# Kernel optimization log

Hardware: AMD Instinct MI355X
Metric: run time of the kernel (lower is better)

The kernel has to match this reference:

```python
import jax, jax.numpy as jnp
import numpy as np

VOCAB, EMBED, HIDDEN = 32000, 256, 512
B, S = 64, 64


def setup_inputs() -> dict:
    key = jax.random.key(0)
    ks = jax.random.split(key, 10)
    target_seq = jax.random.randint(ks[0], (B, S), 0, VOCAB)
    context = jax.random.normal(ks[1], (B, HIDDEN), dtype=jnp.float32)
    h = jax.random.normal(ks[2], (B, HIDDEN), dtype=jnp.float32)
    c = jax.random.normal(ks[3], (B, HIDDEN), dtype=jnp.float32)
    # parameters (torch default-ish init scale)
    emb_table = jax.random.normal(ks[4], (VOCAB, EMBED), dtype=jnp.float32)
    k_lstm = 1.0 / np.sqrt(HIDDEN)
    w_ih = jax.random.uniform(ks[5], (4 * HIDDEN, EMBED + HIDDEN), minval=-k_lstm, maxval=k_lstm, dtype=jnp.float32)
    w_hh = jax.random.uniform(ks[6], (4 * HIDDEN, HIDDEN), minval=-k_lstm, maxval=k_lstm, dtype=jnp.float32)
    b_ih = jax.random.uniform(ks[7], (4 * HIDDEN,), minval=-k_lstm, maxval=k_lstm, dtype=jnp.float32)
    b_hh = jnp.zeros((4 * HIDDEN,), dtype=jnp.float32)
    k_fc = 1.0 / np.sqrt(2 * HIDDEN)
    w_fc = jax.random.uniform(ks[8], (VOCAB, 2 * HIDDEN), minval=-k_fc, maxval=k_fc, dtype=jnp.float32)
    b_fc = jax.random.uniform(ks[9], (VOCAB,), minval=-k_fc, maxval=k_fc, dtype=jnp.float32)
    return dict(target_seq=target_seq, context=context, h=h, c=c,
                emb_table=emb_table, w_ih=w_ih, w_hh=w_hh, b_ih=b_ih, b_hh=b_hh,
                w_fc=w_fc, b_fc=b_fc)


def _decode(target_seq, context, h, c, emb_table, w_ih, w_hh, b_ih, b_hh, w_fc, b_fc):
    # teacher_forcing_ratio = 1.0 -> input at step t is target_seq[:, t]
    emb = emb_table[target_seq]                                    # [B,S,E]
    ctx_t = jnp.broadcast_to(context[:, None, :], (emb.shape[0], emb.shape[1], context.shape[1]))
    lstm_in = jnp.concatenate([emb, ctx_t], axis=-1)               # [B,S,E+H]
    # precompute input-to-hidden part of gates for all steps
    pre = jnp.einsum('bsf,gf->bsg', lstm_in, w_ih) + b_ih + b_hh   # [B,S,4H]
    H = h.shape[1]

    def step(carry, pre_t):
        h_t, c_t = carry
        gates = pre_t + h_t @ w_hh.T                               # [B,4H]
        i, f, g, o = jnp.split(gates, 4, axis=-1)
        i, f, o = jax.nn.sigmoid(i), jax.nn.sigmoid(f), jax.nn.sigmoid(o)
        g = jnp.tanh(g)
        c_n = f * c_t + i * g
        h_n = o * jnp.tanh(c_n)
        return (h_n, c_n), h_n

    _, hs = jax.lax.scan(step, (h, c), jnp.swapaxes(pre, 0, 1))    # hs: [S,B,H]
    hs = jnp.swapaxes(hs, 0, 1)                                    # [B,S,H]
    out_in = jnp.concatenate([hs, ctx_t], axis=-1)                 # [B,S,2H]
    logits = jnp.einsum('bsf,vf->bsv', out_in, w_fc) + b_fc        # [B,S,V]
    return logits


def reference(target_seq, context, h, c, emb_table, w_ih, w_hh, b_ih, b_hh, w_fc, b_fc):
    return _decode(target_seq, context, h, c, emb_table, w_ih, w_hh, b_ih, b_hh, w_fc, b_fc)
```

## Files before the change

### kernel.cpp

```cpp
#include <hip/hip_runtime.h>
#include <hip/hip_bf16.h>

#define VOCAB 32000
#define EMBED 256
#define HIDDEN 512
#define BB 64
#define SS 64
#define M_ROWS (BB * SS)
#define G4 (4 * HIDDEN)
#define NBLK 16

typedef __attribute__((ext_vector_type(8))) short short8v;
typedef __attribute__((ext_vector_type(4))) float float4v;
typedef __attribute__((ext_vector_type(4))) unsigned int uint4v;

__device__ __forceinline__ ushort f2bf(float f) {
    union { float f; unsigned u; } v; v.f = f;
    unsigned r = (v.u + 0x7FFFu + ((v.u >> 16) & 1u)) >> 16;
    return (ushort)r;
}

__device__ __forceinline__ float fast_tanh(float x) {
    float xc = fminf(fmaxf(x, -15.f), 15.f);
    float e = __expf(2.f * xc);
    return (e - 1.f) / (e + 1.f);
}

__device__ __forceinline__ void glds16(const ushort* g, ushort* l) {
    __builtin_amdgcn_global_load_lds(
        (const __attribute__((address_space(1))) unsigned int*)(const void*)g,
        (__attribute__((address_space(3))) unsigned int*)(void*)l, 16, 0, 0);
}

__global__ void k_conv_strided(const float* __restrict__ in, ushort* __restrict__ out,
                               int lg2cols, int instride, int n8) {
    int i = blockIdx.x * blockDim.x + threadIdx.x;
    int stride = gridDim.x * blockDim.x;
    int colmask = (1 << lg2cols) - 1;
    for (; i < n8; i += stride) {
        int i8 = i << 3;
        int row = i8 >> lg2cols, col = i8 & colmask;
        const float* src = in + (size_t)row * instride + col;
        float4 v0 = *(const float4*)src;
        float4 v1 = *(const float4*)(src + 4);
        short8v o;
        o[0] = (short)f2bf(v0.x); o[1] = (short)f2bf(v0.y);
        o[2] = (short)f2bf(v0.z); o[3] = (short)f2bf(v0.w);
        o[4] = (short)f2bf(v1.x); o[5] = (short)f2bf(v1.y);
        o[6] = (short)f2bf(v1.z); o[7] = (short)f2bf(v1.w);
        *(short8v*)(out + i8) = o;
    }
}

__global__ void k_build_emb(const int* __restrict__ tseq, const float* __restrict__ emb,
                            ushort* __restrict__ embbf) {
    int rid = blockIdx.x * 8 + (threadIdx.x >> 5);
    int c0 = (threadIdx.x & 31) * 8;
    int tok = tseq[rid];
    const float* src = emb + (size_t)tok * EMBED + c0;
    float4 v0 = *(const float4*)src;
    float4 v1 = *(const float4*)(src + 4);
    short8v o;
    o[0] = (short)f2bf(v0.x); o[1] = (short)f2bf(v0.y);
    o[2] = (short)f2bf(v0.z); o[3] = (short)f2bf(v0.w);
    o[4] = (short)f2bf(v1.x); o[5] = (short)f2bf(v1.y);
    o[6] = (short)f2bf(v1.z); o[7] = (short)f2bf(v1.w);
    *(short8v*)(embbf + (size_t)rid * EMBED + c0) = o;
}

__global__ void k_prep_small(const float* __restrict__ b_ih, const float* __restrict__ b_hh,
                             float* __restrict__ bias_pre,
                             const float* __restrict__ h0, ushort* __restrict__ hbufA,
                             const float* __restrict__ ctx, ushort* __restrict__ ctx_bf,
                             unsigned* __restrict__ ctrl) {
    int i = blockIdx.x * blockDim.x + threadIdx.x;
    if (i < 256) ctrl[i] = 0;
    if (i < G4) bias_pre[i] = b_ih[i] + b_hh[i];
    if (i < BB * HIDDEN) {
        hbufA[i] = f2bf(h0[i]);
        ctx_bf[i] = f2bf(ctx[i]);
    }
}

__global__ __launch_bounds__(256) void k_gemm_smallM(
    const ushort* __restrict__ Abf, const float* __restrict__ Wf, int wstride,
    const float* __restrict__ bias, float* __restrict__ Cout, int N) {
    int t = threadIdx.x;
    int wv = t >> 6, lane = t & 63, lr = lane & 15, kg = lane >> 4;
    int bcol = blockIdx.x * 128;

    float4v acc[4][2];
#pragma unroll
    for (int m = 0; m < 4; m++)
#pragma unroll
        for (int n = 0; n < 2; n++) acc[m][n] = (float4v){0.f, 0.f, 0.f, 0.f};

#pragma unroll 4
    for (int ks = 0; ks < 16; ks++) {
        short8v a[4];
#pragma unroll
        for (int m = 0; m < 4; m++)
            a[m] = *(const short8v*)(Abf + (size_t)(m * 16 + lr) * 512 + ks * 32 + kg * 8);
        short8v w[2];
#pragma unroll
        for (int n = 0; n < 2; n++) {
            const float* src = Wf + (size_t)(bcol + wv * 32 + n * 16 + lr) * wstride + ks * 32 + kg * 8;
            float4 v0 = *(const float4*)src;
            float4 v1 = *(const float4*)(src + 4);
            short8v w8;
            w8[0] = (short)f2bf(v0.x); w8[1] = (short)f2bf(v0.y);
            w8[2] = (short)f2bf(v0.z); w8[3] = (short)f2bf(v0.w);
            w8[4] = (short)f2bf(v1.x); w8[5] = (short)f2bf(v1.y);
            w8[6] = (short)f2bf(v1.z); w8[7] = (short)f2bf(v1.w);
            w[n] = w8;
        }
#pragma unroll
        for (int m = 0; m < 4; m++)
#pragma unroll
            for (int n = 0; n < 2; n++)
                acc[m][n] = __builtin_amdgcn_mfma_f32_16x16x32_bf16(a[m], w[n], acc[m][n], 0, 0, 0);
    }

#pragma unroll
    for (int n = 0; n < 2; n++) {
        int col = bcol + wv * 32 + n * 16 + lr;
        float bv = bias[col];
#pragma unroll
        for (int m = 0; m < 4; m++) {
            int row = m * 16 + kg * 4;
#pragma unroll
            for (int j = 0; j < 4; j++)
                Cout[(size_t)(row + j) * N + col] = acc[m][n][j] + bv;
        }
    }
}

__global__ __launch_bounds__(512) void k_gemm_bf16(
    const ushort* __restrict__ A, const ushort* __restrict__ W,
    const float* __restrict__ rowbias, float* __restrict__ C,
    int M, int N, int K) {
    __shared__ ushort As[256 * 32];
    __shared__ ushort Ws[256 * 32];
    int t = threadIdx.x;

    int gx = N >> 8, gy = M >> 8;
    int nwg = gx * gy;
    int q = nwg >> 3, r = nwg & 7;
    int xcd = blockIdx.x & 7, idx = blockIdx.x >> 3;
    int wg = (xcd < r) ? xcd * (q + 1) + idx : r * (q + 1) + (xcd - r) * q + idx;
    const int SG = 4;
    int grp = wg / (gx * SG);
    int rem = wg % (gx * SG);
    int bx = rem / SG;
    int by = grp * SG + rem % SG;
    int brow = by * 256, bcol = bx * 256;

    int wave = t >> 6, lane = t & 63;
    int wr = wave >> 2, wc = wave & 3;
    int lr = lane & 15, kg = lane >> 4;

    float4v acc[8][4];
#pragma unroll
    for (int m = 0; m < 8; m++)
#pragma unroll
        for (int n = 0; n < 4; n++) acc[m][n] = (float4v){0.f, 0.f, 0.f, 0.f};

    int srow = t >> 2;
    int scol = (((t & 3) ^ (srow & 3))) * 8;
    const ushort* AgA = A + (size_t)(brow + srow) * K + scol;
    const ushort* AgB = A + (size_t)(brow + 128 + srow) * K + scol;
    const ushort* WgA = W + (size_t)(bcol + srow) * K + scol;
    const ushort* WgB = W + (size_t)(bcol + 128 + srow) * K + scol;
    ushort* ldsA0 = &As[(wave * 16) * 32];
    ushort* ldsA1 = &As[(128 + wave * 16) * 32];
    ushort* ldsW0 = &Ws[(wave * 16) * 32];
    ushort* ldsW1 = &Ws[(128 + wave * 16) * 32];

    for (int bk = 0; bk < K; bk += 32) {
        glds16(AgA + bk, ldsA0);
        glds16(AgB + bk, ldsA1);
        glds16(WgA + bk, ldsW0);
        glds16(WgB + bk, ldsW1);
        __syncthreads();
        short8v a[8], w[4];
#pragma unroll
        for (int m = 0; m < 8; m++) {
            int row = wr * 128 + m * 16 + lr;
            a[m] = *(const short8v*)&As[row * 32 + (kg ^ (row & 3)) * 8];
        }
#pragma unroll
        for (int n = 0; n < 4; n++) {
            int row = wc * 64 + n * 16 + lr;
            w[n] = *(const short8v*)&Ws[row * 32 + (kg ^ (row & 3)) * 8];
        }
#pragma unroll
        for (int m = 0; m < 8; m++)
#pragma unroll
            for (int n = 0; n < 4; n++)
                acc[m][n] = __builtin_amdgcn_mfma_f32_16x16x32_bf16(a[m], w[n], acc[m][n], 0, 0, 0);
        __syncthreads();
    }

#pragma unroll
    for (int n = 0; n < 4; n++) {
        int col = bcol + wc * 64 + n * 16 + lr;
#pragma unroll
        for (int m = 0; m < 8; m++) {
            int row = brow + wr * 128 + m * 16 + kg * 4;
            float bv = rowbias[(size_t)(row >> 6) * N + col];
            float4v v = acc[m][n];
#pragma unroll
            for (int j = 0; j < 4; j++)
                C[(size_t)(row + j) * N + col] = v[j] + bv;
        }
    }
}

__global__ __launch_bounds__(512) void k_lstm(
    const float* __restrict__ pre, const float* __restrict__ w_hh,
    const float* __restrict__ c0,
    ushort* __restrict__ hbufA, ushort* __restrict__ hbufB,
    ushort* __restrict__ out_in, unsigned* __restrict__ flags) {
    __shared__ ushort h_lds[64 * HIDDEN];
    __shared__ float G2[64 * 132];
    int p = blockIdx.x;
    int t = threadIdx.x;
    int w = t >> 6, lane = t & 63, lr = lane & 15, kg = lane >> 4;
    int mh = w >> 2, cw2 = w & 3;

    short8v wfrag[2][16];
#pragma unroll
    for (int ci = 0; ci < 2; ci++) {
        const float* wrow = w_hh + (size_t)(cw2 * HIDDEN + p * 32 + ci * 16 + lr) * HIDDEN;
#pragma unroll
        for (int ks = 0; ks < 16; ks++) {
            const float* src = wrow + ks * 32 + kg * 8;
            short8v w8;
#pragma unroll
            for (int e = 0; e < 8; e++) w8[e] = (short)f2bf(src[e]);
            wfrag[ci][ks] = w8;
        }
    }

    int b = t >> 3, jj0 = (t & 7) * 4, jg0 = p * 32 + jj0;
    float4v c_reg = *(const float4v*)(c0 + (size_t)b * HIDDEN + jg0);
    float4v pv[4];
#pragma unroll
    for (int qg = 0; qg < 4; qg++)
        pv[qg] = *(const float4v*)(pre + (size_t)(b * SS) * G4 + qg * HIDDEN + jg0);

    char* hl = (char*)h_lds;

    for (int s = 0; s < SS; s++) {
        const ushort* hb = (s & 1) ? hbufB : hbufA;
        ushort* hn = (s & 1) ? hbufA : hbufB;

        if (s > 0) {
            const unsigned* fp = flags + (lane & 15) * 16;
            unsigned fv;
            do {
                fv = __hip_atomic_load(fp, __ATOMIC_RELAXED, __HIP_MEMORY_SCOPE_AGENT);
            } while (__all((int)(fv >= (unsigned)s)) == 0);
        }

        {
            uint4v vb[8];
#pragma unroll
            for (int i = 0; i < 8; i++) {
                int rr = w * 8 + i;
                const void* src = hb + (size_t)rr * HIDDEN + lane * 8;
                asm volatile("global_load_dwordx4 %0, %1, off sc0 sc1"
                             : "=&v"(vb[i]) : "v"(src));
            }
            asm volatile("s_waitcnt vmcnt(0)" ::: "memory");
#pragma unroll
            for (int i = 0; i < 8; i++) {
                int rr = w * 8 + i;
                int off = (rr * 1024 + lane * 16) ^ ((rr & 7) << 4);
                *(uint4v*)(hl + off) = vb[i];
            }
        }
        __syncthreads();

        float4v acc[2][2];
#pragma unroll
        for (int mi = 0; mi < 2; mi++)
#pragma unroll
            for (int ci = 0; ci < 2; ci++) acc[mi][ci] = (float4v){0.f, 0.f, 0.f, 0.f};
#pragma unroll
        for (int ks = 0; ks < 16; ks++) {
            short8v a[2];
#pragma unroll
            for (int mi = 0; mi < 2; mi++) {
                int row = mh * 32 + mi * 16 + lr;
                int off = (row * 1024 + ks * 64 + kg * 16) ^ ((row & 7) << 4);
                a[mi] = *(const short8v*)(hl + off);
            }
#pragma unroll
            for (int mi = 0; mi < 2; mi++)
#pragma unroll
                for (int ci = 0; ci < 2; ci++)
                    acc[mi][ci] = __builtin_amdgcn_mfma_f32_16x16x32_bf16(a[mi], wfrag[ci][ks], acc[mi][ci], 0, 0, 0);
        }
#pragma unroll
        for (int mi = 0; mi < 2; mi++)
#pragma unroll
            for (int ci = 0; ci < 2; ci++)
#pragma unroll
                for (int rr = 0; rr < 4; rr++)
                    G2[(mh * 32 + mi * 16 + kg * 4 + rr) * 132 + cw2 * 32 + ci * 16 + lr] = acc[mi][ci][rr];
        __syncthreads();

        {
            float4v gq[4];
#pragma unroll
            for (int qg = 0; qg < 4; qg++) gq[qg] = *(const float4v*)&G2[b * 132 + qg * 32 + jj0];
            unsigned long long hv8 = 0;
#pragma unroll
            for (int e = 0; e < 4; e++) {
                float xi = gq[0][e] + pv[0][e];
                float xf = gq[1][e] + pv[1][e];
                float xg = gq[2][e] + pv[2][e];
                float xo = gq[3][e] + pv[3][e];
                float ig = 1.f / (1.f + __expf(-xi));
                float fg = 1.f / (1.f + __expf(-xf));
                float gg = fast_tanh(xg);
                float og = 1.f / (1.f + __expf(-xo));
                float cn = fg * c_reg[e] + ig * gg;
                float hv = og * fast_tanh(cn);
                c_reg[e] = cn;
                hv8 |= (unsigned long long)f2bf(hv) << (16 * e);
            }
            if (s + 1 < SS) {
                __hip_atomic_store((unsigned long long*)(hn + (size_t)b * HIDDEN + jg0), hv8,
                                   __ATOMIC_RELAXED, __HIP_MEMORY_SCOPE_AGENT);
            }
            *(unsigned long long*)(out_in + (size_t)(b * SS + s) * HIDDEN + jg0) = hv8;
            if (s + 1 < SS) {
#pragma unroll
                for (int qg = 0; qg < 4; qg++)
                    pv[qg] = *(const float4v*)(pre + (size_t)(b * SS + s + 1) * G4 + qg * HIDDEN + jg0);
            }
        }

        __syncthreads();
        if (t == 0 && s + 1 < SS)
            __hip_atomic_store(flags + p * 16, (unsigned)(s + 1),
                               __ATOMIC_RELEASE, __HIP_MEMORY_SCOPE_AGENT);
    }
}

extern "C" void kernel_launch(void* const* d_in, const int* in_sizes, int n_in,
                              void* d_out, int out_size, void* d_ws, size_t ws_size,
                              hipStream_t stream) {
    const int*   tseq = (const int*)d_in[0];
    const float* ctx  = (const float*)d_in[1];
    const float* h0   = (const float*)d_in[2];
    const float* c0   = (const float*)d_in[3];
    const float* emb  = (const float*)d_in[4];
    const float* w_ih = (const float*)d_in[5];
    const float* w_hh = (const float*)d_in[6];
    const float* b_ih = (const float*)d_in[7];
    const float* b_hh = (const float*)d_in[8];
    const float* w_fc = (const float*)d_in[9];
    const float* b_fc = (const float*)d_in[10];
    float* out = (float*)d_out;

    char* wsb = (char*)d_ws;
    size_t off = 0;
    auto alloc = [&](size_t bytes) -> void* {
        void* ptr = wsb + off;
        off = (off + bytes + 255) & ~(size_t)255;
        return ptr;
    };
    ushort* emb_bf    = (ushort*)alloc((size_t)M_ROWS * EMBED * 2);
    ushort* w_ih_ebf  = (ushort*)alloc((size_t)G4 * EMBED * 2);
    ushort* w_fc_hbf  = (ushort*)alloc((size_t)VOCAB * HIDDEN * 2);
    ushort* out_in    = (ushort*)alloc((size_t)M_ROWS * HIDDEN * 2);
    float*  pre       = (float*)alloc((size_t)M_ROWS * G4 * 4);
    float*  prectx    = (float*)alloc((size_t)BB * G4 * 4);
    float*  ctxdot    = (float*)alloc((size_t)BB * VOCAB * 4);
    ushort* ctx_bf    = (ushort*)alloc((size_t)BB * HIDDEN * 2);
    ushort* hbufA     = (ushort*)alloc((size_t)BB * HIDDEN * 2);
    ushort* hbufB     = (ushort*)alloc((size_t)BB * HIDDEN * 2);
    float*  bias_pre  = (float*)alloc((size_t)G4 * 4);
    unsigned* ctrl    = (unsigned*)alloc(1024);

    k_conv_strided<<<256, 256, 0, stream>>>(w_ih, w_ih_ebf, 8, 768, G4 * EMBED / 8);
    k_conv_strided<<<2048, 256, 0, stream>>>(w_fc, w_fc_hbf, 9, 1024, VOCAB * HIDDEN / 8);
    k_build_emb<<<M_ROWS / 8, 256, 0, stream>>>(tseq, emb, emb_bf);
    k_prep_small<<<128, 256, 0, stream>>>(b_ih, b_hh, bias_pre, h0, hbufA, ctx, ctx_bf, ctrl);

    k_gemm_smallM<<<G4 / 128, 256, 0, stream>>>(ctx_bf, w_ih + 256, 768, bias_pre, prectx, G4);
    k_gemm_smallM<<<VOCAB / 128, 256, 0, stream>>>(ctx_bf, w_fc + 512, 1024, b_fc, ctxdot, VOCAB);

    k_gemm_bf16<<<dim3((G4 / 256) * (M_ROWS / 256)), 512, 0, stream>>>(
        emb_bf, w_ih_ebf, prectx, pre, M_ROWS, G4, EMBED);

    void* args[] = {(void*)&pre, (void*)&w_hh, (void*)&c0,
                    (void*)&hbufA, (void*)&hbufB, (void*)&out_in, (void*)&ctrl};
    hipLaunchCooperativeKernel((void*)k_lstm, dim3(NBLK), dim3(512), args, 0, stream);

    k_gemm_bf16<<<dim3((VOCAB / 256) * (M_ROWS / 256)), 512, 0, stream>>>(
        out_in, w_fc_hbf, ctxdot, out, M_ROWS, VOCAB, HIDDEN);
}
```

Measured before the change: 799.5 us.

## Fuse LSTM recurrence and output projection into one persistent cooperative kernel

Merges the sequential LSTM kernel and the vocabulary projection GEMM into a single cooperative launch of 256 blocks. The first 16 blocks run the recurrence while the rest pull output tiles from an atomic work queue, waiting on per-step flags before each tile. To make a 256-row tile correspond to 4 complete time steps, out_in is now laid out step-major, which lets the projection start while later steps are still being computed. The cost is spin-waiting blocks that compete for memory bandwidth with the latency-bound recurrence, plus a strided scatter of the output in the epilogue.

```diff
diff --git a/kernel.cpp b/kernel.cpp
--- a/kernel.cpp
+++ b/kernel.cpp
@@ -9,6 +9,9 @@
 #define M_ROWS (BB * SS)
 #define G4 (4 * HIDDEN)
 #define NBLK 16
+#define NTOT 256
+#define NTILE_N (VOCAB / 256)
+#define NTILE_M (M_ROWS / 256)
 
 typedef __attribute__((ext_vector_type(8))) short short8v;
 typedef __attribute__((ext_vector_type(4))) float float4v;
@@ -74,7 +77,7 @@
                              const float* __restrict__ ctx, ushort* __restrict__ ctx_bf,
                              unsigned* __restrict__ ctrl) {
     int i = blockIdx.x * blockDim.x + threadIdx.x;
-    if (i < 256) ctrl[i] = 0;
+    if (i < 1024) ctrl[i] = 0;
     if (i < G4) bias_pre[i] = b_ih[i] + b_hh[i];
     if (i < BB * HIDDEN) {
         hbufA[i] = f2bf(h0[i]);
@@ -216,137 +219,237 @@
     }
 }
 
-__global__ __launch_bounds__(512) void k_lstm(
+__global__ __launch_bounds__(512) void k_mega(
     const float* __restrict__ pre, const float* __restrict__ w_hh,
     const float* __restrict__ c0,
     ushort* __restrict__ hbufA, ushort* __restrict__ hbufB,
-    ushort* __restrict__ out_in, unsigned* __restrict__ flags) {
-    __shared__ ushort h_lds[64 * HIDDEN];
-    __shared__ float G2[64 * 132];
-    int p = blockIdx.x;
+    ushort* __restrict__ out_in, unsigned* __restrict__ ctrl,
+    const ushort* __restrict__ Wfc, const float* __restrict__ ctxdot,
+    float* __restrict__ Cout) {
+    __shared__ __align__(16) char smem[99328];
+    __shared__ int s_tile;
+    unsigned* flags = ctrl;
+    unsigned* queue = ctrl + 512;
     int t = threadIdx.x;
-    int w = t >> 6, lane = t & 63, lr = lane & 15, kg = lane >> 4;
-    int mh = w >> 2, cw2 = w & 3;
-
-    short8v wfrag[2][16];
-#pragma unroll
-    for (int ci = 0; ci < 2; ci++) {
-        const float* wrow = w_hh + (size_t)(cw2 * HIDDEN + p * 32 + ci * 16 + lr) * HIDDEN;
-#pragma unroll
-        for (int ks = 0; ks < 16; ks++) {
-            const float* src = wrow + ks * 32 + kg * 8;
-            short8v w8;
-#pragma unroll
-            for (int e = 0; e < 8; e++) w8[e] = (short)f2bf(src[e]);
-            wfrag[ci][ks] = w8;
-        }
-    }
-
-    int b = t >> 3, jj0 = (t & 7) * 4, jg0 = p * 32 + jj0;
-    float4v c_reg = *(const float4v*)(c0 + (size_t)b * HIDDEN + jg0);
-    float4v pv[4];
-#pragma unroll
-    for (int qg = 0; qg < 4; qg++)
-        pv[qg] = *(const float4v*)(pre + (size_t)(b * SS) * G4 + qg * HIDDEN + jg0);
-
-    char* hl = (char*)h_lds;
-
-    for (int s = 0; s < SS; s++) {
-        const ushort* hb = (s & 1) ? hbufB : hbufA;
-        ushort* hn = (s & 1) ? hbufA : hbufB;
-
-        if (s > 0) {
-            const unsigned* fp = flags + (lane & 15) * 16;
-            unsigned fv;
-            do {
-                fv = __hip_atomic_load(fp, __ATOMIC_RELAXED, __HIP_MEMORY_SCOPE_AGENT);
-            } while (__all((int)(fv >= (unsigned)s)) == 0);
-        }
-
-        {
-            uint4v vb[8];
-#pragma unroll
-            for (int i = 0; i < 8; i++) {
-                int rr = w * 8 + i;
-                const void* src = hb + (size_t)rr * HIDDEN + lane * 8;
+    int bid = blockIdx.x;
+    int wave = t >> 6, lane = t & 63, lr = lane & 15, kg = lane >> 4;
+
+    if (bid < NBLK) {
+        ushort* h_lds = (ushort*)smem;
+        float* G2 = (float*)(smem + 65536);
+        char* hl = (char*)h_lds;
+        int p = bid;
+        int w = wave;
+        int mh = w >> 2, cw2 = w & 3;
+
+        short8v wfrag[2][16];
+#pragma unroll
+        for (int ci = 0; ci < 2; ci++) {
+            const float* wrow = w_hh + (size_t)(cw2 * HIDDEN + p * 32 + ci * 16 + lr) * HIDDEN;
+#pragma unroll
+            for (int ks = 0; ks < 16; ks++) {
+                const float* src = wrow + ks * 32 + kg * 8;
+                short8v w8;
+#pragma unroll
+                for (int e = 0; e < 8; e++) w8[e] = (short)f2bf(src[e]);
+                wfrag[ci][ks] = w8;
+            }
+        }
+
+        int b = t >> 3, jj0 = (t & 7) * 4, jg0 = p * 32 + jj0;
+        float4v c_reg = *(const float4v*)(c0 + (size_t)b * HIDDEN + jg0);
+        float4v pv[4];
+#pragma unroll
+        for (int qg = 0; qg < 4; qg++)
+            pv[qg] = *(const float4v*)(pre + (size_t)(b * SS) * G4 + qg * HIDDEN + jg0);
+
+        for (int s = 0; s < SS; s++) {
+            const ushort* hb = (s & 1) ? hbufB : hbufA;
+            ushort* hn = (s & 1) ? hbufA : hbufB;
+
+            if (s > 0) {
+                const unsigned* fp = flags + (lane & 15) * 16;
+                unsigned fv;
+                do {
+                    fv = __hip_atomic_load(fp, __ATOMIC_RELAXED, __HIP_MEMORY_SCOPE_AGENT);
+                } while (__all((int)(fv >= (unsigned)s)) == 0);
+            }
+
+            {
+                uint4v vb[8];
+#pragma unroll
+                for (int i = 0; i < 8; i++) {
+                    int rr = w * 8 + i;
+                    const void* src = hb + (size_t)rr * HIDDEN + lane * 8;
+                    asm volatile("global_load_dwordx4 %0, %1, off sc0 sc1"
+                                 : "=&v"(vb[i]) : "v"(src));
+                }
+                asm volatile("s_waitcnt vmcnt(0)" ::: "memory");
+#pragma unroll
+                for (int i = 0; i < 8; i++) {
+                    int rr = w * 8 + i;
+                    int off = (rr * 1024 + lane * 16) ^ ((rr & 7) << 4);
+                    *(uint4v*)(hl + off) = vb[i];
+                }
+            }
+            __syncthreads();
+
+            float4v acc[2][2];
+#pragma unroll
+            for (int mi = 0; mi < 2; mi++)
+#pragma unroll
+                for (int ci = 0; ci < 2; ci++) acc[mi][ci] = (float4v){0.f, 0.f, 0.f, 0.f};
+#pragma unroll
+            for (int ks = 0; ks < 16; ks++) {
+                short8v a[2];
+#pragma unroll
+                for (int mi = 0; mi < 2; mi++) {
+                    int row = mh * 32 + mi * 16 + lr;
+                    int off = (row * 1024 + ks * 64 + kg * 16) ^ ((row & 7) << 4);
+                    a[mi] = *(const short8v*)(hl + off);
+                }
+#pragma unroll
+                for (int mi = 0; mi < 2; mi++)
+#pragma unroll
+                    for (int ci = 0; ci < 2; ci++)
+                        acc[mi][ci] = __builtin_amdgcn_mfma_f32_16x16x32_bf16(a[mi], wfrag[ci][ks], acc[mi][ci], 0, 0, 0);
+            }
+#pragma unroll
+            for (int mi = 0; mi < 2; mi++)
+#pragma unroll
+                for (int ci = 0; ci < 2; ci++)
+#pragma unroll
+                    for (int rr = 0; rr < 4; rr++)
+                        G2[(mh * 32 + mi * 16 + kg * 4 + rr) * 132 + cw2 * 32 + ci * 16 + lr] = acc[mi][ci][rr];
+            __syncthreads();
+
+            {
+                float4v gq[4];
+#pragma unroll
+                for (int qg = 0; qg < 4; qg++) gq[qg] = *(const float4v*)&G2[b * 132 + qg * 32 + jj0];
+                unsigned long long hv8 = 0;
+#pragma unroll
+                for (int e = 0; e < 4; e++) {
+                    float xi = gq[0][e] + pv[0][e];
+                    float xf = gq[1][e] + pv[1][e];
+                    float xg = gq[2][e] + pv[2][e];
+                    float xo = gq[3][e] + pv[3][e];
+                    float ig = 1.f / (1.f + __expf(-xi));
+                    float fg = 1.f / (1.f + __expf(-xf));
+                    float gg = fast_tanh(xg);
+                    float og = 1.f / (1.f + __expf(-xo));
+                    float cn = fg * c_reg[e] + ig * gg;
+                    float hv = og * fast_tanh(cn);
+                    c_reg[e] = cn;
+                    hv8 |= (unsigned long long)f2bf(hv) << (16 * e);
+                }
+                if (s + 1 < SS) {
+                    __hip_atomic_store((unsigned long long*)(hn + (size_t)b * HIDDEN + jg0), hv8,
+                                       __ATOMIC_RELAXED, __HIP_MEMORY_SCOPE_AGENT);
+                }
+                __hip_atomic_store((unsigned long long*)(out_in + (size_t)(s * BB + b) * HIDDEN + jg0), hv8,
+                                   __ATOMIC_RELAXED, __HIP_MEMORY_SCOPE_AGENT);
+                if (s + 1 < SS) {
+#pragma unroll
+                    for (int qg = 0; qg < 4; qg++)
+                        pv[qg] = *(const float4v*)(pre + (size_t)(b * SS + s + 1) * G4 + qg * HIDDEN + jg0);
+                }
+            }
+
+            __syncthreads();
+            if (t == 0)
+                __hip_atomic_store(flags + p * 16, (unsigned)(s + 1),
+                                   __ATOMIC_RELEASE, __HIP_MEMORY_SCOPE_AGENT);
+        }
+    } else {
+        ushort* As = (ushort*)smem;
+        ushort* Ws = (ushort*)(smem + 16384);
+        int wr = wave >> 2, wc = wave & 3;
+        int srow = t >> 2;
+        int scolU = ((t & 3) ^ (srow & 3)) * 8;
+        int aoff0 = srow * 64 + (t & 3) * 16;
+        int aoff1 = aoff0 + 128 * 64;
+        ushort* ldsW0 = Ws + (wave * 16) * 32;
+        ushort* ldsW1 = Ws + (128 + wave * 16) * 32;
+
+        for (;;) {
+            __syncthreads();
+            if (t == 0)
+                s_tile = (int)__hip_atomic_fetch_add(queue, 1u, __ATOMIC_RELAXED, __HIP_MEMORY_SCOPE_AGENT);
+            __syncthreads();
+            int tile = s_tile;
+            if (tile >= NTILE_M * NTILE_N) break;
+            int mt = tile / NTILE_N, nt = tile % NTILE_N;
+            int brow = mt * 256, bcol = nt * 256;
+
+            {
+                unsigned need = (unsigned)(4 * mt + 4);
+                const unsigned* fp = flags + (lane & 15) * 16;
+                unsigned fv;
+                do {
+                    fv = __hip_atomic_load(fp, __ATOMIC_RELAXED, __HIP_MEMORY_SCOPE_AGENT);
+                } while (__all((int)(fv >= need)) == 0);
+            }
+
+            float4v acc[8][4];
+#pragma unroll
+            for (int m = 0; m < 8; m++)
+#pragma unroll
+                for (int n = 0; n < 4; n++) acc[m][n] = (float4v){0.f, 0.f, 0.f, 0.f};
+
+            const ushort* Arow0 = out_in + (size_t)(brow + srow) * HIDDEN + scolU;
+            const ushort* Arow1 = Arow0 + (size_t)128 * HIDDEN;
+            const ushort* WgA = Wfc + (size_t)(bcol + srow) * HIDDEN + scolU;
+            const ushort* WgB = WgA + (size_t)128 * HIDDEN;
+
+            for (int bk = 0; bk < HIDDEN; bk += 32) {
+                uint4v va0, va1;
                 asm volatile("global_load_dwordx4 %0, %1, off sc0 sc1"
-                             : "=&v"(vb[i]) : "v"(src));
-            }
-            asm volatile("s_waitcnt vmcnt(0)" ::: "memory");
-#pragma unroll
-            for (int i = 0; i < 8; i++) {
-                int rr = w * 8 + i;
-                int off = (rr * 1024 + lane * 16) ^ ((rr & 7) << 4);
-                *(uint4v*)(hl + off) = vb[i];
-            }
-        }
-        __syncthreads();
-
-        float4v acc[2][2];
-#pragma unroll
-        for (int mi = 0; mi < 2; mi++)
-#pragma unroll
-            for (int ci = 0; ci < 2; ci++) acc[mi][ci] = (float4v){0.f, 0.f, 0.f, 0.f};
-#pragma unroll
-        for (int ks = 0; ks < 16; ks++) {
-            short8v a[2];
-#pragma unroll
-            for (int mi = 0; mi < 2; mi++) {
-                int row = mh * 32 + mi * 16 + lr;
-                int off = (row * 1024 + ks * 64 + kg * 16) ^ ((row & 7) << 4);
-                a[mi] = *(const short8v*)(hl + off);
-            }
-#pragma unroll
-            for (int mi = 0; mi < 2; mi++)
-#pragma unroll
-                for (int ci = 0; ci < 2; ci++)
-                    acc[mi][ci] = __builtin_amdgcn_mfma_f32_16x16x32_bf16(a[mi], wfrag[ci][ks], acc[mi][ci], 0, 0, 0);
-        }
-#pragma unroll
-        for (int mi = 0; mi < 2; mi++)
-#pragma unroll
-            for (int ci = 0; ci < 2; ci++)
-#pragma unroll
-                for (int rr = 0; rr < 4; rr++)
-                    G2[(mh * 32 + mi * 16 + kg * 4 + rr) * 132 + cw2 * 32 + ci * 16 + lr] = acc[mi][ci][rr];
-        __syncthreads();
-
-        {
-            float4v gq[4];
-#pragma unroll
-            for (int qg = 0; qg < 4; qg++) gq[qg] = *(const float4v*)&G2[b * 132 + qg * 32 + jj0];
-            unsigned long long hv8 = 0;
-#pragma unroll
-            for (int e = 0; e < 4; e++) {
-                float xi = gq[0][e] + pv[0][e];
-                float xf = gq[1][e] + pv[1][e];
-                float xg = gq[2][e] + pv[2][e];
-                float xo = gq[3][e] + pv[3][e];
-                float ig = 1.f / (1.f + __expf(-xi));
-                float fg = 1.f / (1.f + __expf(-xf));
-                float gg = fast_tanh(xg);
-                float og = 1.f / (1.f + __expf(-xo));
-                float cn = fg * c_reg[e] + ig * gg;
-                float hv = og * fast_tanh(cn);
-                c_reg[e] = cn;
-                hv8 |= (unsigned long long)f2bf(hv) << (16 * e);
-            }
-            if (s + 1 < SS) {
-                __hip_atomic_store((unsigned long long*)(hn + (size_t)b * HIDDEN + jg0), hv8,
-                                   __ATOMIC_RELAXED, __HIP_MEMORY_SCOPE_AGENT);
-            }
-            *(unsigned long long*)(out_in + (size_t)(b * SS + s) * HIDDEN + jg0) = hv8;
-            if (s + 1 < SS) {
-#pragma unroll
-                for (int qg = 0; qg < 4; qg++)
-                    pv[qg] = *(const float4v*)(pre + (size_t)(b * SS + s + 1) * G4 + qg * HIDDEN + jg0);
-            }
-        }
-
-        __syncthreads();
-        if (t == 0 && s + 1 < SS)
-            __hip_atomic_store(flags + p * 16, (unsigned)(s + 1),
-                               __ATOMIC_RELEASE, __HIP_MEMORY_SCOPE_AGENT);
+                             : "=&v"(va0) : "v"((const void*)(Arow0 + bk)));
+                asm volatile("global_load_dwordx4 %0, %1, off sc0 sc1"
+                             : "=&v"(va1) : "v"((const void*)(Arow1 + bk)));
+                glds16(WgA + bk, ldsW0);
+                glds16(WgB + bk, ldsW1);
+                asm volatile("s_waitcnt vmcnt(2)" ::: "memory");
+                *(uint4v*)((char*)As + aoff0) = va0;
+                *(uint4v*)((char*)As + aoff1) = va1;
+                __syncthreads();
+                short8v a[8], w[4];
+#pragma unroll
+                for (int m = 0; m < 8; m++) {
+                    int row = wr * 128 + m * 16 + lr;
+                    a[m] = *(const short8v*)&As[row * 32 + (kg ^ (row & 3)) * 8];
+                }
+#pragma unroll
+                for (int n = 0; n < 4; n++) {
+                    int row = wc * 64 + n * 16 + lr;
+                    w[n] = *(const short8v*)&Ws[row * 32 + (kg ^ (row & 3)) * 8];
+                }
+#pragma unroll
+                for (int m = 0; m < 8; m++)
+#pragma unroll
+                    for (int n = 0; n < 4; n++)
+                        acc[m][n] = __builtin_amdgcn_mfma_f32_16x16x32_bf16(a[m], w[n], acc[m][n], 0, 0, 0);
+                __syncthreads();
+            }
+
+#pragma unroll
+            for (int n = 0; n < 4; n++) {
+                int col = bcol + wc * 64 + n * 16 + lr;
+#pragma unroll
+                for (int m = 0; m < 8; m++) {
+                    int rbase = wr * 128 + m * 16 + kg * 4;
+#pragma unroll
+                    for (int j = 0; j < 4; j++) {
+                        int rl = rbase + j;
+                        int bb = rl & 63;
+                        int ss = mt * 4 + (rl >> 6);
+                        Cout[(size_t)(bb * 64 + ss) * VOCAB + col] =
+                            acc[m][n][j] + ctxdot[(size_t)bb * VOCAB + col];
+                    }
+                }
+            }
+        }
     }
 }
 
@@ -384,7 +487,7 @@
     ushort* hbufA     = (ushort*)alloc((size_t)BB * HIDDEN * 2);
     ushort* hbufB     = (ushort*)alloc((size_t)BB * HIDDEN * 2);
     float*  bias_pre  = (float*)alloc((size_t)G4 * 4);
-    unsigned* ctrl    = (unsigned*)alloc(1024);
+    unsigned* ctrl    = (unsigned*)alloc(4096);
 
     k_conv_strided<<<256, 256, 0, stream>>>(w_ih, w_ih_ebf, 8, 768, G4 * EMBED / 8);
     k_conv_strided<<<2048, 256, 0, stream>>>(w_fc, w_fc_hbf, 9, 1024, VOCAB * HIDDEN / 8);
@@ -398,9 +501,7 @@
         emb_bf, w_ih_ebf, prectx, pre, M_ROWS, G4, EMBED);
 
     void* args[] = {(void*)&pre, (void*)&w_hh, (void*)&c0,
-                    (void*)&hbufA, (void*)&hbufB, (void*)&out_in, (void*)&ctrl};
-    hipLaunchCooperativeKernel((void*)k_lstm, dim3(NBLK), dim3(512), args, 0, stream);
-
-    k_gemm_bf16<<<dim3((VOCAB / 256) * (M_ROWS / 256)), 512, 0, stream>>>(
-        out_in, w_fc_hbf, ctxdot, out, M_ROWS, VOCAB, HIDDEN);
-}
+                    (void*)&hbufA, (void*)&hbufB, (void*)&out_in, (void*)&ctrl,
+                    (void*)&w_fc_hbf, (void*)&ctxdot, (void*)&out};
+    hipLaunchCooperativeKernel((void*)k_mega, dim3(NTOT), dim3(512), args, 0, stream);
+}
```

Result: faster. 673.5 us (-15.8%).
